# Kernel tuning notes

Measured on AMD Instinct MI355X. Metric: run time of the kernel, lower is better.

## Reference

```python
import jax, jax.numpy as jnp
import numpy as np

S, B, D, H, FF = 1024, 8, 512, 8, 2048
HD = D // H
ALPHA, BETA = 0.5, 0.5
EPS = 1e-5


def setup_inputs() -> dict:
    key = jax.random.key(0)
    ks = jax.random.split(key, 12)
    rn = lambda k, sh, sc=0.02: jax.random.normal(k, sh, dtype=jnp.float32) * sc
    ln = jnp.stack([jnp.ones(D), jnp.zeros(D), jnp.ones(D), jnp.zeros(D)]).astype(jnp.float32)
    return {
        "src": rn(ks[0], (S, B, D), 1.0),
        "src_depth": rn(ks[1], (S, B, D), 1.0),
        "pos": rn(ks[2], (S, B, D), 1.0),
        "attn_w_img": rn(ks[3], (4, D, D)),
        "attn_b_img": jnp.zeros((4, D), jnp.float32),
        "attn_w_dpt": rn(ks[4], (4, D, D)),
        "attn_b_dpt": jnp.zeros((4, D), jnp.float32),
        "ffn_w1_img": rn(ks[5], (FF, D)),
        "ffn_b1_img": jnp.zeros((FF,), jnp.float32),
        "ffn_w2_img": rn(ks[6], (D, FF)),
        "ffn_b2_img": jnp.zeros((D,), jnp.float32),
        "ffn_w1_dpt": rn(ks[7], (FF, D)),
        "ffn_b1_dpt": jnp.zeros((FF,), jnp.float32),
        "ffn_w2_dpt": rn(ks[8], (D, FF)),
        "ffn_b2_dpt": jnp.zeros((D,), jnp.float32),
        "ln_img": ln,
        "ln_dpt": ln,
    }


def _layer_norm(x, g, b):
    m = jnp.mean(x, axis=-1, keepdims=True)
    v = jnp.var(x, axis=-1, keepdims=True)  # biased, matches torch LayerNorm
    return (x - m) * jax.lax.rsqrt(v + EPS) * g + b


def _heads(t, W, b):  # [B,S,D] x [D,D] -> [B,H,S,hd]  (torch Linear: y = x W^T + b)
    y = jnp.einsum('bsd,ed->bse', t, W) + b
    return y.reshape(B, S, H, HD).transpose(0, 2, 1, 3)


def _forward(src, src_depth, pos, attn_w_img, attn_b_img, attn_w_dpt, attn_b_dpt,
             ffn_w1_img, ffn_b1_img, ffn_w2_img, ffn_b2_img,
             ffn_w1_dpt, ffn_b1_dpt, ffn_w2_dpt, ffn_b2_dpt, ln_img, ln_dpt):
    # seq-first -> batch-first
    x = src.transpose(1, 0, 2)        # [B,S,D]
    xd = src_depth.transpose(1, 0, 2)
    p = pos.transpose(1, 0, 2)
    qk_in = x + p                     # img stream: q = k = src + pos
    # depth stream: pos_depth is None in layer.forward -> no pos embed
    q = _heads(qk_in, attn_w_img[0], attn_b_img[0])
    k = _heads(qk_in, attn_w_img[1], attn_b_img[1])
    v = _heads(x, attn_w_img[2], attn_b_img[2])
    qd = _heads(xd, attn_w_dpt[0], attn_b_dpt[0])
    kd = _heads(xd, attn_w_dpt[1], attn_b_dpt[1])
    vd = _heads(xd, attn_w_dpt[2], attn_b_dpt[2])
    scale = 1.0 / np.sqrt(HD).astype(np.float32)
    a_img = jax.nn.softmax(jnp.einsum('bhld,bhsd->bhls', q, k) * scale, axis=-1)
    a_dpt = jax.nn.softmax(jnp.einsum('bhld,bhsd->bhls', qd, kd) * scale, axis=-1)
    sh_img = (1.0 - ALPHA) * a_img + ALPHA * a_dpt
    sh_dpt = (1.0 - BETA) * a_dpt + BETA * a_img
    o_img = jnp.einsum('bhls,bhsd->bhld', sh_img, v).transpose(0, 2, 1, 3).reshape(B, S, D)
    o_dpt = jnp.einsum('bhls,bhsd->bhld', sh_dpt, vd).transpose(0, 2, 1, 3).reshape(B, S, D)
    o_img = jnp.einsum('bsd,ed->bse', o_img, attn_w_img[3]) + attn_b_img[3]
    o_dpt = jnp.einsum('bsd,ed->bse', o_dpt, attn_w_dpt[3]) + attn_b_dpt[3]
    # img residual + LN + FFN + LN
    x = _layer_norm(x + o_img, ln_img[0], ln_img[1])
    ff = jnp.einsum('bsf,df->bsd',
                    jax.nn.relu(jnp.einsum('bsd,fd->bsf', x, ffn_w1_img) + ffn_b1_img),
                    ffn_w2_img) + ffn_b2_img
    x = _layer_norm(x + ff, ln_img[2], ln_img[3])
    # depth residual + LN + FFN + LN
    xd = _layer_norm(xd + o_dpt, ln_dpt[0], ln_dpt[1])
    ffd = jnp.einsum('bsf,df->bsd',
                     jax.nn.relu(jnp.einsum('bsd,fd->bsf', xd, ffn_w1_dpt) + ffn_b1_dpt),
                     ffn_w2_dpt) + ffn_b2_dpt
    xd = _layer_norm(xd + ffd, ln_dpt[2], ln_dpt[3])
    return x.transpose(1, 0, 2), xd.transpose(1, 0, 2)  # back to [S,B,D]


def reference(src, src_depth, pos, attn_w_img, attn_b_img, attn_w_dpt, attn_b_dpt,
              ffn_w1_img, ffn_b1_img, ffn_w2_img, ffn_b2_img,
              ffn_w1_dpt, ffn_b1_dpt, ffn_w2_dpt, ffn_b2_dpt, ln_img, ln_dpt):
    return _forward(src, src_depth, pos, attn_w_img, attn_b_img, attn_w_dpt, attn_b_dpt,
                    ffn_w1_img, ffn_b1_img, ffn_w2_img, ffn_b2_img,
                    ffn_w1_dpt, ffn_b1_dpt, ffn_w2_dpt, ffn_b2_dpt, ln_img, ln_dpt)
```

## Files before the change

kernel.cpp:

```cpp
#include <hip/hip_runtime.h>
#include <math.h>

#define S_  1024
#define B_  8
#define D_  512
#define H_  8
#define HD_ 64
#define FF_ 2048
#define M_  8192
#define DD_ (D_ * D_)

typedef __attribute__((ext_vector_type(8))) short short8;
typedef __attribute__((ext_vector_type(4))) float f32x4;

static __device__ __forceinline__ unsigned short f2bf(float x) {
  union { float f; unsigned int u; } v; v.f = x;
  unsigned int r = v.u + 0x7fff + ((v.u >> 16) & 1);
  return (unsigned short)(r >> 16);
}
static __device__ __forceinline__ float bf2f(unsigned short x) {
  union { unsigned int u; float f; } v; v.u = ((unsigned int)x) << 16;
  return v.f;
}
static __device__ __forceinline__ unsigned int pack_bf2(float a, float b) {
  union { float f; unsigned int u; } x, y; x.f = a; y.f = b;
  return ((x.u + 0x8000u) >> 16) | ((y.u + 0x8000u) & 0xffff0000u);
}
static __device__ __forceinline__ void gl_lds16(const unsigned short* g, unsigned short* l) {
  __builtin_amdgcn_global_load_lds((__attribute__((address_space(1))) void*)(g),
                                   (__attribute__((address_space(3))) void*)(l), 16, 0, 0);
}
static __device__ __forceinline__ int xcd_swz(int phys, int nwg) {
  int cpx = nwg >> 3;
  return (phys & 7) * cpx + (phys >> 3);
}

struct CvtJobs { const float* in[6]; unsigned short* out[6]; };
__global__ __launch_bounds__(256) void wcvt_kernel(CvtJobs j) {
  int job = blockIdx.y;
  int i = (blockIdx.x * 256 + threadIdx.x) * 4;
  float4 v = *(const float4*)(j.in[job] + i);
  unsigned short u[4] = {f2bf(v.x), f2bf(v.y), f2bf(v.z), f2bf(v.w)};
  *(uint2*)(j.out[job] + i) = *(const uint2*)u;
}

__global__ __launch_bounds__(256) void acvt_kernel(const float* __restrict__ src,
    const float* __restrict__ srcd, const float* __restrict__ pos,
    unsigned short* __restrict__ src16, unsigned short* __restrict__ srcd16,
    unsigned short* __restrict__ qkin16) {
  int job = blockIdx.y;
  int i = (blockIdx.x * 256 + threadIdx.x) * 4;
  const float* a = (job == 0) ? src : (job == 1) ? srcd : src;
  float4 v = *(const float4*)(a + i);
  if (job == 2) {
    float4 p = *(const float4*)(pos + i);
    v.x += p.x; v.y += p.y; v.z += p.z; v.w += p.w;
  }
  unsigned short* o = (job == 0) ? src16 : (job == 1) ? srcd16 : qkin16;
  unsigned short u[4] = {f2bf(v.x), f2bf(v.y), f2bf(v.z), f2bf(v.w)};
  *(uint2*)(o + i) = *(const uint2*)u;
}

static __device__ __forceinline__ void mgemm_body(
    const unsigned short* __restrict__ X, const unsigned short* __restrict__ W,
    const float* __restrict__ bias, const float* __restrict__ resf,
    const unsigned short* __restrict__ resb, unsigned short* __restrict__ Yb,
    float* __restrict__ Yf, int N, int K, int relu, int bx, int by,
    unsigned short* As, unsigned short* Bs)
{
  int tid = threadIdx.x;
  int lane = tid & 63, w = tid >> 6;
  int ml = lane & 15, g = lane >> 4;
  int wm = w >> 1, wn = w & 1;
  int m0 = by * 128, n0 = bx * 128;

  int lrow = tid >> 3;
  int lcol = ((tid & 7) ^ (lrow & 7)) * 8;
  const unsigned short* gA = X + (size_t)(m0 + lrow) * K + lcol;
  const unsigned short* gB = W + (size_t)(n0 + lrow) * K + lcol;
  unsigned short* lA = As + w * 512;
  unsigned short* lB = Bs + w * 512;

  f32x4 acc[4][4];
  #pragma unroll
  for (int i = 0; i < 4; i++)
    #pragma unroll
    for (int j = 0; j < 4; j++) acc[i][j] = (f32x4){0.f, 0.f, 0.f, 0.f};

  int NT = K >> 6;

  auto STAGE = [&](int buf, int kt) {
    const unsigned short* ga = gA + kt * 64;
    const unsigned short* gb = gB + kt * 64;
    unsigned short* la = lA + buf * 8192;
    unsigned short* lb = lB + buf * 8192;
    #pragma unroll
    for (int rr = 0; rr < 4; rr++) {
      gl_lds16(ga + (size_t)rr * 32 * K, la + rr * 2048);
      gl_lds16(gb + (size_t)rr * 32 * K, lb + rr * 2048);
    }
  };

  STAGE(0, 0);
  if (NT > 1) STAGE(1, 1);

  for (int kt = 0; kt < NT; kt++) {
    int cur = kt & 1;
    if (kt + 1 < NT) {
      asm volatile("s_waitcnt vmcnt(8)" ::: "memory");
    } else {
      asm volatile("s_waitcnt vmcnt(0)" ::: "memory");
    }
    __builtin_amdgcn_sched_barrier(0);
    __builtin_amdgcn_s_barrier();

    const unsigned short* lAc = As + cur * 8192;
    const unsigned short* lBc = Bs + cur * 8192;
    short8 af[2][4], bfr[2][4];
    #pragma unroll
    for (int ks = 0; ks < 2; ks++) {
      #pragma unroll
      for (int i = 0; i < 4; i++) {
        int r = wm * 64 + i * 16 + ml;
        af[ks][i] = *(const short8*)&lAc[r * 64 + (((ks * 4 + g) ^ (r & 7)) * 8)];
      }
      #pragma unroll
      for (int j = 0; j < 4; j++) {
        int r = wn * 64 + j * 16 + ml;
        bfr[ks][j] = *(const short8*)&lBc[r * 64 + (((ks * 4 + g) ^ (r & 7)) * 8)];
      }
    }
    asm volatile("s_waitcnt lgkmcnt(0)" ::: "memory");
    __builtin_amdgcn_sched_barrier(0);
    __builtin_amdgcn_s_barrier();
    if (kt + 2 < NT) STAGE(cur, kt + 2);
    __builtin_amdgcn_sched_barrier(0);

    #pragma unroll
    for (int ks = 0; ks < 2; ks++)
      #pragma unroll
      for (int i = 0; i < 4; i++)
        #pragma unroll
        for (int j = 0; j < 4; j++)
          acc[i][j] = __builtin_amdgcn_mfma_f32_16x16x32_bf16(af[ks][i], bfr[ks][j], acc[i][j], 0, 0, 0);
  }

  #pragma unroll
  for (int i = 0; i < 4; i++) {
    int grow = m0 + wm * 64 + i * 16 + g * 4;
    #pragma unroll
    for (int j = 0; j < 4; j++) {
      int gcol = n0 + wn * 64 + j * 16 + ml;
      float bv = bias[gcol];
      #pragma unroll
      for (int r = 0; r < 4; r++) {
        size_t idx = (size_t)(grow + r) * N + gcol;
        float v = acc[i][j][r] + bv;
        if (resf) v += resf[idx];
        if (resb) v += bf2f(resb[idx]);
        if (relu) v = fmaxf(v, 0.0f);
        if (Yb) Yb[idx] = f2bf(v);
        if (Yf) Yf[idx] = v;
      }
    }
  }
}

__global__ __launch_bounds__(256) void qkv_kernel(
    const unsigned short* __restrict__ qkin, const unsigned short* __restrict__ src16,
    const unsigned short* __restrict__ srcd16,
    const unsigned short* __restrict__ w_i, const unsigned short* __restrict__ w_d,
    const float* __restrict__ bA_i, const float* __restrict__ bA_d,
    unsigned short* __restrict__ qkimg, unsigned short* __restrict__ vimg,
    unsigned short* __restrict__ dptqkv)
{
  __shared__ unsigned short As[2 * 128 * 64];
  __shared__ unsigned short Bs[2 * 128 * 64];
  int phys = blockIdx.x + 24 * blockIdx.y;
  int L = xcd_swz(phys, 24 * 64);
  int bx = L % 24, by = L / 24;
  if (bx < 8)
    mgemm_body(qkin, w_i, bA_i, nullptr, nullptr, qkimg, nullptr, 1024, 512, 0, bx, by, As, Bs);
  else if (bx < 12)
    mgemm_body(src16, w_i + 2 * DD_, bA_i + 1024, nullptr, nullptr, vimg, nullptr, 512, 512, 0, bx - 8, by, As, Bs);
  else
    mgemm_body(srcd16, w_d, bA_d, nullptr, nullptr, dptqkv, nullptr, 1536, 512, 0, bx - 12, by, As, Bs);
}

__global__ __launch_bounds__(256) void pgemm_kernel(
    const unsigned short* __restrict__ X0, const unsigned short* __restrict__ X1,
    const unsigned short* __restrict__ W0, const unsigned short* __restrict__ W1,
    const float* __restrict__ b0, const float* __restrict__ b1,
    const float* __restrict__ rf0, const float* __restrict__ rf1,
    const unsigned short* __restrict__ rb0, const unsigned short* __restrict__ rb1,
    unsigned short* __restrict__ Y0, unsigned short* __restrict__ Y1,
    int N, int K, int relu)
{
  __shared__ unsigned short As[2 * 128 * 64];
  __shared__ unsigned short Bs[2 * 128 * 64];
  int nbx = gridDim.x;
  int nwg = nbx * 64 * 2;
  int phys = blockIdx.x + nbx * (blockIdx.y + 64 * blockIdx.z);
  int L = xcd_swz(phys, nwg);
  int bx = L % nbx; int rem = L / nbx;
  int by = rem % 64; int z = rem / 64;
  mgemm_body(z ? X1 : X0, z ? W1 : W0, z ? b1 : b0, z ? rf1 : rf0,
             z ? rb1 : rb0, z ? Y1 : Y0, nullptr, N, K, relu,
             bx, by, As, Bs);
}

__global__ __launch_bounds__(256) void vtrans_kernel(
    const unsigned short* __restrict__ v0, int ld0, unsigned short* __restrict__ vt0,
    const unsigned short* __restrict__ v1, int ld1, unsigned short* __restrict__ vt1)
{
  __shared__ unsigned short tile[64][72];
  const unsigned short* v = blockIdx.z ? v1 : v0;
  unsigned short* vt = blockIdx.z ? vt1 : vt0;
  int ld = blockIdx.z ? ld1 : ld0;
  int bh = blockIdx.y, b = bh >> 3, h = bh & 7;
  int s0 = blockIdx.x * 64;
  int tid = threadIdx.x;
  #pragma unroll
  for (int t = 0; t < 2; t++) {
    int idx = t * 256 + tid;
    int i = idx >> 3, c8 = (idx & 7) * 8;
    *(uint4*)&tile[i][c8] =
        *(const uint4*)(v + ((size_t)(s0 + i) * B_ + b) * ld + h * HD_ + c8);
  }
  __syncthreads();
  int hd = tid >> 2, j0 = (tid & 3) * 16;
  unsigned short tmp[16];
  #pragma unroll
  for (int j = 0; j < 16; j++) tmp[j] = tile[j0 + j][hd];
  unsigned short* dst = vt + ((size_t)bh * HD_ + hd) * S_ + s0 + j0;
  *(uint4*)(dst) = *(const uint4*)&tmp[0];
  *(uint4*)(dst + 8) = *(const uint4*)&tmp[8];
}

__global__ __launch_bounds__(256) void ln16_kernel(
    const unsigned short* __restrict__ X0, const unsigned short* __restrict__ X1,
    unsigned short* __restrict__ Yb0, unsigned short* __restrict__ Yb1,
    float* __restrict__ Yf0, float* __restrict__ Yf1,
    const float* __restrict__ gb0, const float* __restrict__ gb1)
{
  int row = blockIdx.x, tid = threadIdx.x;
  int strm = row >> 13, r = row & 8191;
  const unsigned short* X = strm ? X1 : X0;
  unsigned short* Yb = strm ? Yb1 : Yb0;
  float* Yf = strm ? Yf1 : Yf0;
  const float* gb = strm ? gb1 : gb0;

  ushort2 xv = *(const ushort2*)(X + (size_t)r * D_ + 2 * tid);
  float v0 = bf2f(xv.x), v1 = bf2f(xv.y);
  float s = v0 + v1, q = v0 * v0 + v1 * v1;
  #pragma unroll
  for (int msk = 1; msk < 64; msk <<= 1) {
    s += __shfl_xor(s, msk);
    q += __shfl_xor(q, msk);
  }
  __shared__ float ss[4], qs[4];
  int wid = tid >> 6;
  if ((tid & 63) == 0) { ss[wid] = s; qs[wid] = q; }
  __syncthreads();
  s = ss[0] + ss[1] + ss[2] + ss[3];
  q = qs[0] + qs[1] + qs[2] + qs[3];
  float mean = s * (1.0f / D_);
  float var  = q * (1.0f / D_) - mean * mean;
  float inv  = rsqrtf(var + 1e-5f);
  float2 gg = *(const float2*)(gb + 2 * tid);
  float2 bb = *(const float2*)(gb + 512 + 2 * tid);
  float o0 = (v0 - mean) * inv * gg.x + bb.x;
  float o1 = (v1 - mean) * inv * gg.y + bb.y;
  if (Yb) {
    unsigned int pk = pack_bf2(o0, o1);
    unsigned short u[2] = {f2bf(o0), f2bf(o1)};
    *(unsigned int*)(Yb + (size_t)r * D_ + 2 * tid) = *(const unsigned int*)u;
    (void)pk;
  }
  if (Yf) {
    float2 o; o.x = o0; o.y = o1;
    *(float2*)(Yf + (size_t)r * D_ + 2 * tid) = o;
  }
}

__global__ __launch_bounds__(256, 2) void attn_kernel(
    const unsigned short* __restrict__ Qi, const unsigned short* __restrict__ Ki, int ldi,
    const unsigned short* __restrict__ Vti,
    const unsigned short* __restrict__ Qd, const unsigned short* __restrict__ Kd, int ldd,
    const unsigned short* __restrict__ Vtd,
    unsigned short* __restrict__ oi, unsigned short* __restrict__ od)
{
  __shared__ __align__(16) unsigned short Kls[2][64 * 64];
  __shared__ __align__(16) unsigned short Vls[2][64 * 64];
  __shared__ __align__(16) unsigned short Pl[4][2][16 * 72];

  int tid = threadIdx.x;
  int phys = blockIdx.x + 8 * blockIdx.y;
  int L = xcd_swz(phys, 8 * 64);
  int bh = L >> 3, b = bh >> 3, h = bh & 7;
  int q0 = (L & 7) * 128;
  int lane = tid & 63, w = tid >> 6;
  int ml = lane & 15, g = lane >> 4;
  int mx = ml & 7;

  short8 qf[2][2][2];
  #pragma unroll
  for (int t = 0; t < 2; t++) {
    size_t tok = (size_t)(q0 + w * 32 + t * 16 + ml) * B_ + b;
    const unsigned short* qa_i = Qi + tok * ldi + h * HD_ + g * 8;
    const unsigned short* qa_d = Qd + tok * ldd + h * HD_ + g * 8;
    qf[t][0][0] = *(const short8*)(qa_i);  qf[t][0][1] = *(const short8*)(qa_i + 32);
    qf[t][1][0] = *(const short8*)(qa_d);  qf[t][1][1] = *(const short8*)(qa_d + 32);
  }

  int srow = lane >> 3;
  int chg = (lane & 7) ^ srow;
  const unsigned short* gbase; size_t s1, s2; unsigned short* lbase;
  if (w == 0)      { gbase = Ki  + ((size_t)srow * B_ + b) * ldi + h * HD_ + chg * 8; s1 = (size_t)B_ * ldi; s2 = s1; lbase = &Kls[0][0]; }
  else if (w == 1) { gbase = Kd  + ((size_t)srow * B_ + b) * ldd + h * HD_ + chg * 8; s1 = (size_t)B_ * ldd; s2 = s1; lbase = &Kls[1][0]; }
  else if (w == 2) { gbase = Vti + (size_t)bh * HD_ * S_ + (size_t)srow * S_ + chg * 8; s1 = S_; s2 = 1; lbase = &Vls[0][0]; }
  else             { gbase = Vtd + (size_t)bh * HD_ * S_ + (size_t)srow * S_ + chg * 8; s1 = S_; s2 = 1; lbase = &Vls[1][0]; }

  f32x4 acc4[2][4][4];
  #pragma unroll
  for (int t = 0; t < 2; t++)
    #pragma unroll
    for (int cb = 0; cb < 4; cb++)
      #pragma unroll
      for (int n = 0; n < 4; n++) acc4[t][cb][n] = (f32x4){0.f, 0.f, 0.f, 0.f};
  float lI[2] = {0.f, 0.f}, lD[2] = {0.f, 0.f};
  const float scale = 0.125f;

  for (int kt = 0; kt < S_ / 64; kt++) {
    int k0 = kt * 64;
    __syncthreads();
    {
      const unsigned short* gp = gbase + (size_t)k0 * s2;
      #pragma unroll
      for (int rr = 0; rr < 8; rr++)
        gl_lds16(gp + (size_t)rr * 8 * s1, lbase + rr * 512);
    }
    __syncthreads();

    #pragma unroll
    for (int t = 0; t < 2; t++) {
      #pragma unroll
      for (int st = 0; st < 2; st++) {
        float* ls = st ? &lD[t] : &lI[t];
        const unsigned short* Kt = &Kls[st][0];
        #pragma unroll
        for (int n = 0; n < 4; n++) {
          int rbase = (n * 16 + ml) * 64;
          short8 kf0 = *(const short8*)&Kt[rbase + ((g ^ mx) * 8)];
          short8 kf1 = *(const short8*)&Kt[rbase + (((g + 4) ^ mx) * 8)];
          f32x4 a = (f32x4){0.f, 0.f, 0.f, 0.f};
          a = __builtin_amdgcn_mfma_f32_16x16x32_bf16(kf0, qf[t][st][0], a, 0, 0, 0);
          a = __builtin_amdgcn_mfma_f32_16x16x32_bf16(kf1, qf[t][st][1], a, 0, 0, 0);
          float p0 = __expf(a[0] * scale), p1 = __expf(a[1] * scale);
          float p2 = __expf(a[2] * scale), p3 = __expf(a[3] * scale);
          *ls += (p0 + p1) + (p2 + p3);
          uint2 pk; pk.x = pack_bf2(p0, p1); pk.y = pack_bf2(p2, p3);
          *(uint2*)&Pl[w][st][ml * 72 + n * 16 + g * 4] = pk;
        }
      }
      #pragma unroll
      for (int c = 0; c < 2; c++) {
        short8 pI = *(const short8*)&Pl[w][0][ml * 72 + g * 8 + c * 32];
        short8 pD = *(const short8*)&Pl[w][1][ml * 72 + g * 8 + c * 32];
        #pragma unroll
        for (int n = 0; n < 4; n++) {
          int rbase = (n * 16 + ml) * 64;
          int sc = (((g + 4 * c) ^ mx)) * 8;
          short8 vI = *(const short8*)&Vls[0][rbase + sc];
          short8 vD = *(const short8*)&Vls[1][rbase + sc];
          acc4[t][0][n] = __builtin_amdgcn_mfma_f32_16x16x32_bf16(pI, vI, acc4[t][0][n], 0, 0, 0);
          acc4[t][1][n] = __builtin_amdgcn_mfma_f32_16x16x32_bf16(pD, vI, acc4[t][1][n], 0, 0, 0);
          acc4[t][2][n] = __builtin_amdgcn_mfma_f32_16x16x32_bf16(pI, vD, acc4[t][2][n], 0, 0, 0);
          acc4[t][3][n] = __builtin_amdgcn_mfma_f32_16x16x32_bf16(pD, vD, acc4[t][3][n], 0, 0, 0);
        }
      }
    }
  }

  #pragma unroll
  for (int t = 0; t < 2; t++) {
    lI[t] += __shfl_xor(lI[t], 16);  lI[t] += __shfl_xor(lI[t], 32);
    lD[t] += __shfl_xor(lD[t], 16);  lD[t] += __shfl_xor(lD[t], 32);
  }
  #pragma unroll
  for (int t = 0; t < 2; t++) {
    float invI = 1.0f / lI[t], invD = 1.0f / lD[t];
    #pragma unroll
    for (int r = 0; r < 4; r++) {
      float iI = __shfl(invI, g * 4 + r, 16);
      float iD = __shfl(invD, g * 4 + r, 16);
      int qrow = q0 + w * 32 + t * 16 + g * 4 + r;
      size_t ob = ((size_t)qrow * B_ + b) * D_ + h * HD_;
      #pragma unroll
      for (int n = 0; n < 4; n++) {
        oi[ob + n * 16 + ml] = f2bf(0.5f * (acc4[t][0][n][r] * iI + acc4[t][1][n][r] * iD));
        od[ob + n * 16 + ml] = f2bf(0.5f * (acc4[t][3][n][r] * iD + acc4[t][2][n][r] * iI));
      }
    }
  }
}

extern "C" void kernel_launch(void* const* d_in, const int* in_sizes, int n_in,
                              void* d_out, int out_size, void* d_ws, size_t ws_size,
                              hipStream_t stream) {
  const float* src  = (const float*)d_in[0];
  const float* srcd = (const float*)d_in[1];
  const float* pos  = (const float*)d_in[2];
  const float* wA_i = (const float*)d_in[3];
  const float* bA_i = (const float*)d_in[4];
  const float* wA_d = (const float*)d_in[5];
  const float* bA_d = (const float*)d_in[6];
  const float* w1_i = (const float*)d_in[7];
  const float* b1_i = (const float*)d_in[8];
  const float* w2_i = (const float*)d_in[9];
  const float* b2_i = (const float*)d_in[10];
  const float* w1_d = (const float*)d_in[11];
  const float* b1_d = (const float*)d_in[12];
  const float* w2_d = (const float*)d_in[13];
  const float* b2_d = (const float*)d_in[14];
  const float* ln_i = (const float*)d_in[15];
  const float* ln_d = (const float*)d_in[16];

  float* out = (float*)d_out;
  unsigned short* u = (unsigned short*)d_ws;
  const size_t T4 = (size_t)M_ * D_;
  const size_t WSZ = (size_t)FF_ * D_;

  unsigned short* src16  = u;
  unsigned short* srcd16 = u + T4;
  unsigned short* qkimg  = u + 2 * T4;
  unsigned short* vimg   = u + 4 * T4;
  unsigned short* dptqkv = u + 5 * T4;
  unsigned short* w_i16  = u + 8 * T4;
  unsigned short* w_d16  = w_i16 + WSZ;
  unsigned short* w1i16  = w_d16 + WSZ;
  unsigned short* w2i16  = w1i16 + WSZ;
  unsigned short* w1d16  = w2i16 + WSZ;
  unsigned short* w2d16  = w1d16 + WSZ;
  unsigned short* t16_i  = w2d16 + WSZ;
  unsigned short* t16_d  = t16_i + T4;
  unsigned short* x16_i  = t16_d + T4;
  unsigned short* x16_d  = x16_i + T4;
  unsigned short* vt_i   = src16;
  unsigned short* vt_d   = srcd16;
  unsigned short* h16_i  = u;
  unsigned short* h16_d  = u + 4 * T4;
  unsigned short* qkin16 = (unsigned short*)out;
  unsigned short* oi16   = (unsigned short*)out;
  unsigned short* od16   = (unsigned short*)out + T4;

  dim3 blk(256);

  CvtJobs cj;
  cj.in[0] = wA_i; cj.out[0] = w_i16;
  cj.in[1] = wA_d; cj.out[1] = w_d16;
  cj.in[2] = w1_i; cj.out[2] = w1i16;
  cj.in[3] = w2_i; cj.out[3] = w2i16;
  cj.in[4] = w1_d; cj.out[4] = w1d16;
  cj.in[5] = w2_d; cj.out[5] = w2d16;
  wcvt_kernel<<<dim3(1024, 6), blk, 0, stream>>>(cj);
  acvt_kernel<<<dim3(4096, 3), blk, 0, stream>>>(src, srcd, pos, src16, srcd16, qkin16);

  qkv_kernel<<<dim3(24, 64), blk, 0, stream>>>(qkin16, src16, srcd16, w_i16, w_d16,
                                               bA_i, bA_d, qkimg, vimg, dptqkv);
  vtrans_kernel<<<dim3(16, 64, 2), blk, 0, stream>>>(vimg, 512, vt_i, dptqkv + 1024, 1536, vt_d);

  attn_kernel<<<dim3(S_ / 128, B_ * H_), blk, 0, stream>>>(
      qkimg, qkimg + 512, 1024, vt_i, dptqkv, dptqkv + 512, 1536, vt_d, oi16, od16);

  pgemm_kernel<<<dim3(4, 64, 2), blk, 0, stream>>>(
      oi16, od16, w_i16 + 3 * DD_, w_d16 + 3 * DD_, bA_i + 1536, bA_d + 1536,
      src, srcd, nullptr, nullptr, t16_i, t16_d, 512, 512, 0);
  ln16_kernel<<<2 * M_, blk, 0, stream>>>(t16_i, t16_d, x16_i, x16_d,
                                          nullptr, nullptr, ln_i, ln_d);
  pgemm_kernel<<<dim3(16, 64, 2), blk, 0, stream>>>(
      x16_i, x16_d, w1i16, w1d16, b1_i, b1_d,
      nullptr, nullptr, nullptr, nullptr, h16_i, h16_d, 2048, 512, 1);
  pgemm_kernel<<<dim3(4, 64, 2), blk, 0, stream>>>(
      h16_i, h16_d, w2i16, w2d16, b2_i, b2_d,
      nullptr, nullptr, x16_i, x16_d, t16_i, t16_d, 512, 2048, 0);
  ln16_kernel<<<2 * M_, blk, 0, stream>>>(t16_i, t16_d, nullptr, nullptr,
                                          out, out + T4, ln_i + 2 * D_, ln_d + 2 * D_);
}
```

Baseline: 434.1 us.

## Double-buffer V tiles and overlap next K/V load with PV MFMAs

```diff
diff --git a/kernel.cpp b/kernel.cpp
--- a/kernel.cpp
+++ b/kernel.cpp
@@ -291,7 +291,7 @@
     unsigned short* __restrict__ oi, unsigned short* __restrict__ od)
 {
   __shared__ __align__(16) unsigned short Kls[2][64 * 64];
-  __shared__ __align__(16) unsigned short Vls[2][64 * 64];
+  __shared__ __align__(16) unsigned short Vls[2][2][64 * 64];
   __shared__ __align__(16) unsigned short Pl[4][2][16 * 72];
 
   int tid = threadIdx.x;
@@ -315,11 +315,11 @@
 
   int srow = lane >> 3;
   int chg = (lane & 7) ^ srow;
-  const unsigned short* gbase; size_t s1, s2; unsigned short* lbase;
-  if (w == 0)      { gbase = Ki  + ((size_t)srow * B_ + b) * ldi + h * HD_ + chg * 8; s1 = (size_t)B_ * ldi; s2 = s1; lbase = &Kls[0][0]; }
-  else if (w == 1) { gbase = Kd  + ((size_t)srow * B_ + b) * ldd + h * HD_ + chg * 8; s1 = (size_t)B_ * ldd; s2 = s1; lbase = &Kls[1][0]; }
-  else if (w == 2) { gbase = Vti + (size_t)bh * HD_ * S_ + (size_t)srow * S_ + chg * 8; s1 = S_; s2 = 1; lbase = &Vls[0][0]; }
-  else             { gbase = Vtd + (size_t)bh * HD_ * S_ + (size_t)srow * S_ + chg * 8; s1 = S_; s2 = 1; lbase = &Vls[1][0]; }
+  const unsigned short* gbase; size_t s1, s2;
+  if (w == 0)      { gbase = Ki  + ((size_t)srow * B_ + b) * ldi + h * HD_ + chg * 8; s1 = (size_t)B_ * ldi; s2 = s1; }
+  else if (w == 1) { gbase = Kd  + ((size_t)srow * B_ + b) * ldd + h * HD_ + chg * 8; s1 = (size_t)B_ * ldd; s2 = s1; }
+  else if (w == 2) { gbase = Vti + (size_t)bh * HD_ * S_ + (size_t)srow * S_ + chg * 8; s1 = S_; s2 = 1; }
+  else             { gbase = Vtd + (size_t)bh * HD_ * S_ + (size_t)srow * S_ + chg * 8; s1 = S_; s2 = 1; }
 
   f32x4 acc4[2][4][4];
   #pragma unroll
@@ -331,55 +331,70 @@
   float lI[2] = {0.f, 0.f}, lD[2] = {0.f, 0.f};
   const float scale = 0.125f;
 
+  auto stage_kv = [&](int kt, int buf) {
+    unsigned short* lb;
+    if (w == 0)      lb = &Kls[0][0];
+    else if (w == 1) lb = &Kls[1][0];
+    else if (w == 2) lb = &Vls[buf][0][0];
+    else             lb = &Vls[buf][1][0];
+    const unsigned short* gp = gbase + (size_t)(kt * 64) * s2;
+    #pragma unroll
+    for (int rr = 0; rr < 8; rr++)
+      gl_lds16(gp + (size_t)rr * 8 * s1, lb + rr * 512);
+  };
+
+  auto qk_phase = [&](int t) {
+    #pragma unroll
+    for (int st = 0; st < 2; st++) {
+      float* ls = st ? &lD[t] : &lI[t];
+      const unsigned short* Kt = &Kls[st][0];
+      #pragma unroll
+      for (int n = 0; n < 4; n++) {
+        int rbase = (n * 16 + ml) * 64;
+        short8 kf0 = *(const short8*)&Kt[rbase + ((g ^ mx) * 8)];
+        short8 kf1 = *(const short8*)&Kt[rbase + (((g + 4) ^ mx) * 8)];
+        f32x4 a = (f32x4){0.f, 0.f, 0.f, 0.f};
+        a = __builtin_amdgcn_mfma_f32_16x16x32_bf16(kf0, qf[t][st][0], a, 0, 0, 0);
+        a = __builtin_amdgcn_mfma_f32_16x16x32_bf16(kf1, qf[t][st][1], a, 0, 0, 0);
+        float p0 = __expf(a[0] * scale), p1 = __expf(a[1] * scale);
+        float p2 = __expf(a[2] * scale), p3 = __expf(a[3] * scale);
+        *ls += (p0 + p1) + (p2 + p3);
+        uint2 pk; pk.x = pack_bf2(p0, p1); pk.y = pack_bf2(p2, p3);
+        *(uint2*)&Pl[w][st][ml * 72 + n * 16 + g * 4] = pk;
+      }
+    }
+  };
+
+  auto pv_phase = [&](int t, int p) {
+    #pragma unroll
+    for (int c = 0; c < 2; c++) {
+      short8 pI = *(const short8*)&Pl[w][0][ml * 72 + g * 8 + c * 32];
+      short8 pD = *(const short8*)&Pl[w][1][ml * 72 + g * 8 + c * 32];
+      #pragma unroll
+      for (int n = 0; n < 4; n++) {
+        int rbase = (n * 16 + ml) * 64;
+        int sc = (((g + 4 * c) ^ mx)) * 8;
+        short8 vI = *(const short8*)&Vls[p][0][rbase + sc];
+        short8 vD = *(const short8*)&Vls[p][1][rbase + sc];
+        acc4[t][0][n] = __builtin_amdgcn_mfma_f32_16x16x32_bf16(pI, vI, acc4[t][0][n], 0, 0, 0);
+        acc4[t][1][n] = __builtin_amdgcn_mfma_f32_16x16x32_bf16(pD, vI, acc4[t][1][n], 0, 0, 0);
+        acc4[t][2][n] = __builtin_amdgcn_mfma_f32_16x16x32_bf16(pI, vD, acc4[t][2][n], 0, 0, 0);
+        acc4[t][3][n] = __builtin_amdgcn_mfma_f32_16x16x32_bf16(pD, vD, acc4[t][3][n], 0, 0, 0);
+      }
+    }
+  };
+
+  stage_kv(0, 0);
+
   for (int kt = 0; kt < S_ / 64; kt++) {
-    int k0 = kt * 64;
+    int p = kt & 1;
     __syncthreads();
-    {
-      const unsigned short* gp = gbase + (size_t)k0 * s2;
-      #pragma unroll
-      for (int rr = 0; rr < 8; rr++)
-        gl_lds16(gp + (size_t)rr * 8 * s1, lbase + rr * 512);
-    }
+    qk_phase(0);
+    pv_phase(0, p);
+    qk_phase(1);
     __syncthreads();
-
-    #pragma unroll
-    for (int t = 0; t < 2; t++) {
-      #pragma unroll
-      for (int st = 0; st < 2; st++) {
-        float* ls = st ? &lD[t] : &lI[t];
-        const unsigned short* Kt = &Kls[st][0];
-        #pragma unroll
-        for (int n = 0; n < 4; n++) {
-          int rbase = (n * 16 + ml) * 64;
-          short8 kf0 = *(const short8*)&Kt[rbase + ((g ^ mx) * 8)];
-          short8 kf1 = *(const short8*)&Kt[rbase + (((g + 4) ^ mx) * 8)];
-          f32x4 a = (f32x4){0.f, 0.f, 0.f, 0.f};
-          a = __builtin_amdgcn_mfma_f32_16x16x32_bf16(kf0, qf[t][st][0], a, 0, 0, 0);
-          a = __builtin_amdgcn_mfma_f32_16x16x32_bf16(kf1, qf[t][st][1], a, 0, 0, 0);
-          float p0 = __expf(a[0] * scale), p1 = __expf(a[1] * scale);
-          float p2 = __expf(a[2] * scale), p3 = __expf(a[3] * scale);
-          *ls += (p0 + p1) + (p2 + p3);
-          uint2 pk; pk.x = pack_bf2(p0, p1); pk.y = pack_bf2(p2, p3);
-          *(uint2*)&Pl[w][st][ml * 72 + n * 16 + g * 4] = pk;
-        }
-      }
-      #pragma unroll
-      for (int c = 0; c < 2; c++) {
-        short8 pI = *(const short8*)&Pl[w][0][ml * 72 + g * 8 + c * 32];
-        short8 pD = *(const short8*)&Pl[w][1][ml * 72 + g * 8 + c * 32];
-        #pragma unroll
-        for (int n = 0; n < 4; n++) {
-          int rbase = (n * 16 + ml) * 64;
-          int sc = (((g + 4 * c) ^ mx)) * 8;
-          short8 vI = *(const short8*)&Vls[0][rbase + sc];
-          short8 vD = *(const short8*)&Vls[1][rbase + sc];
-          acc4[t][0][n] = __builtin_amdgcn_mfma_f32_16x16x32_bf16(pI, vI, acc4[t][0][n], 0, 0, 0);
-          acc4[t][1][n] = __builtin_amdgcn_mfma_f32_16x16x32_bf16(pD, vI, acc4[t][1][n], 0, 0, 0);
-          acc4[t][2][n] = __builtin_amdgcn_mfma_f32_16x16x32_bf16(pI, vD, acc4[t][2][n], 0, 0, 0);
-          acc4[t][3][n] = __builtin_amdgcn_mfma_f32_16x16x32_bf16(pD, vD, acc4[t][3][n], 0, 0, 0);
-        }
-      }
-    }
+    if (kt + 1 < S_ / 64) stage_kv(kt + 1, p ^ 1);
+    pv_phase(1, p);
   }
 
   #pragma unroll
```

Result: slower. 607.6 us (+40.0%).

## Shrink GEMM K-tile to 32 with simpler double buffering and higher occupancy

Applied to the files above, without the earlier changes.

```diff
diff --git a/kernel.cpp b/kernel.cpp
--- a/kernel.cpp
+++ b/kernel.cpp
@@ -73,11 +73,12 @@
   int ml = lane & 15, g = lane >> 4;
   int wm = w >> 1, wn = w & 1;
   int m0 = by * 128, n0 = bx * 128;
-
-  int lrow = tid >> 3;
-  int lcol = ((tid & 7) ^ (lrow & 7)) * 8;
-  const unsigned short* gA = X + (size_t)(m0 + lrow) * K + lcol;
-  const unsigned short* gB = W + (size_t)(n0 + lrow) * K + lcol;
+  int mxs = (ml >> 1) & 3;
+
+  int lrow = tid >> 2;
+  int sg = (tid & 3) ^ ((lrow >> 1) & 3);
+  const unsigned short* gA = X + (size_t)(m0 + lrow) * K + sg * 8;
+  const unsigned short* gB = W + (size_t)(n0 + lrow) * K + sg * 8;
   unsigned short* lA = As + w * 512;
   unsigned short* lB = Bs + w * 512;
 
@@ -87,62 +88,46 @@
     #pragma unroll
     for (int j = 0; j < 4; j++) acc[i][j] = (f32x4){0.f, 0.f, 0.f, 0.f};
 
-  int NT = K >> 6;
+  int NT = K >> 5;
 
   auto STAGE = [&](int buf, int kt) {
-    const unsigned short* ga = gA + kt * 64;
-    const unsigned short* gb = gB + kt * 64;
-    unsigned short* la = lA + buf * 8192;
-    unsigned short* lb = lB + buf * 8192;
-    #pragma unroll
-    for (int rr = 0; rr < 4; rr++) {
-      gl_lds16(ga + (size_t)rr * 32 * K, la + rr * 2048);
-      gl_lds16(gb + (size_t)rr * 32 * K, lb + rr * 2048);
-    }
+    const unsigned short* ga = gA + kt * 32;
+    const unsigned short* gb = gB + kt * 32;
+    unsigned short* la = lA + buf * 4096;
+    unsigned short* lb = lB + buf * 4096;
+    gl_lds16(ga, la);
+    gl_lds16(ga + (size_t)64 * K, la + 2048);
+    gl_lds16(gb, lb);
+    gl_lds16(gb + (size_t)64 * K, lb + 2048);
   };
 
   STAGE(0, 0);
-  if (NT > 1) STAGE(1, 1);
+  __syncthreads();
 
   for (int kt = 0; kt < NT; kt++) {
     int cur = kt & 1;
-    if (kt + 1 < NT) {
-      asm volatile("s_waitcnt vmcnt(8)" ::: "memory");
-    } else {
-      asm volatile("s_waitcnt vmcnt(0)" ::: "memory");
-    }
-    __builtin_amdgcn_sched_barrier(0);
-    __builtin_amdgcn_s_barrier();
-
-    const unsigned short* lAc = As + cur * 8192;
-    const unsigned short* lBc = Bs + cur * 8192;
-    short8 af[2][4], bfr[2][4];
-    #pragma unroll
-    for (int ks = 0; ks < 2; ks++) {
-      #pragma unroll
-      for (int i = 0; i < 4; i++) {
-        int r = wm * 64 + i * 16 + ml;
-        af[ks][i] = *(const short8*)&lAc[r * 64 + (((ks * 4 + g) ^ (r & 7)) * 8)];
-      }
-      #pragma unroll
-      for (int j = 0; j < 4; j++) {
-        int r = wn * 64 + j * 16 + ml;
-        bfr[ks][j] = *(const short8*)&lBc[r * 64 + (((ks * 4 + g) ^ (r & 7)) * 8)];
-      }
-    }
-    asm volatile("s_waitcnt lgkmcnt(0)" ::: "memory");
-    __builtin_amdgcn_sched_barrier(0);
-    __builtin_amdgcn_s_barrier();
-    if (kt + 2 < NT) STAGE(cur, kt + 2);
-    __builtin_amdgcn_sched_barrier(0);
-
-    #pragma unroll
-    for (int ks = 0; ks < 2; ks++)
-      #pragma unroll
-      for (int i = 0; i < 4; i++)
-        #pragma unroll
-        for (int j = 0; j < 4; j++)
-          acc[i][j] = __builtin_amdgcn_mfma_f32_16x16x32_bf16(af[ks][i], bfr[ks][j], acc[i][j], 0, 0, 0);
+    if (kt + 1 < NT) STAGE(cur ^ 1, kt + 1);
+
+    const unsigned short* lAc = As + cur * 4096;
+    const unsigned short* lBc = Bs + cur * 4096;
+    short8 af[4], bfr[4];
+    #pragma unroll
+    for (int i = 0; i < 4; i++) {
+      int r = wm * 64 + i * 16 + ml;
+      af[i] = *(const short8*)&lAc[r * 32 + ((g ^ mxs) * 8)];
+    }
+    #pragma unroll
+    for (int j = 0; j < 4; j++) {
+      int r = wn * 64 + j * 16 + ml;
+      bfr[j] = *(const short8*)&lBc[r * 32 + ((g ^ mxs) * 8)];
+    }
+    #pragma unroll
+    for (int i = 0; i < 4; i++)
+      #pragma unroll
+      for (int j = 0; j < 4; j++)
+        acc[i][j] = __builtin_amdgcn_mfma_f32_16x16x32_bf16(af[i], bfr[j], acc[i][j], 0, 0, 0);
+
+    __syncthreads();
   }
 
   #pragma unroll
@@ -166,7 +151,7 @@
   }
 }
 
-__global__ __launch_bounds__(256) void qkv_kernel(
+__global__ __launch_bounds__(256, 4) void qkv_kernel(
     const unsigned short* __restrict__ qkin, const unsigned short* __restrict__ src16,
     const unsigned short* __restrict__ srcd16,
     const unsigned short* __restrict__ w_i, const unsigned short* __restrict__ w_d,
@@ -174,8 +159,8 @@
     unsigned short* __restrict__ qkimg, unsigned short* __restrict__ vimg,
     unsigned short* __restrict__ dptqkv)
 {
-  __shared__ unsigned short As[2 * 128 * 64];
-  __shared__ unsigned short Bs[2 * 128 * 64];
+  __shared__ unsigned short As[2 * 128 * 32];
+  __shared__ unsigned short Bs[2 * 128 * 32];
   int phys = blockIdx.x + 24 * blockIdx.y;
   int L = xcd_swz(phys, 24 * 64);
   int bx = L % 24, by = L / 24;
@@ -187,7 +172,7 @@
     mgemm_body(srcd16, w_d, bA_d, nullptr, nullptr, dptqkv, nullptr, 1536, 512, 0, bx - 12, by, As, Bs);
 }
 
-__global__ __launch_bounds__(256) void pgemm_kernel(
+__global__ __launch_bounds__(256, 4) void pgemm_kernel(
     const unsigned short* __restrict__ X0, const unsigned short* __restrict__ X1,
     const unsigned short* __restrict__ W0, const unsigned short* __restrict__ W1,
     const float* __restrict__ b0, const float* __restrict__ b1,
@@ -196,8 +181,8 @@
     unsigned short* __restrict__ Y0, unsigned short* __restrict__ Y1,
     int N, int K, int relu)
 {
-  __shared__ unsigned short As[2 * 128 * 64];
-  __shared__ unsigned short Bs[2 * 128 * 64];
+  __shared__ unsigned short As[2 * 128 * 32];
+  __shared__ unsigned short Bs[2 * 128 * 32];
   int nbx = gridDim.x;
   int nwg = nbx * 64 * 2;
   int phys = blockIdx.x + nbx * (blockIdx.y + 64 * blockIdx.z);
@@ -272,10 +257,8 @@
   float o0 = (v0 - mean) * inv * gg.x + bb.x;
   float o1 = (v1 - mean) * inv * gg.y + bb.y;
   if (Yb) {
-    unsigned int pk = pack_bf2(o0, o1);
     unsigned short u[2] = {f2bf(o0), f2bf(o1)};
     *(unsigned int*)(Yb + (size_t)r * D_ + 2 * tid) = *(const unsigned int*)u;
-    (void)pk;
   }
   if (Yf) {
     float2 o; o.x = o0; o.y = o1;
```

Result: no change. 434.2 us (+0.0%).
